# Optimization experiments

Hardware: AMD Instinct MI355X
Metric: run time of the kernel (lower is better)

## Reference

```python
import jax, jax.numpy as jnp
import numpy as np

N_CODES = 8192
EMBED_DIM = 64
N_VOXELS = 32768


def setup_inputs() -> dict:
    key = jax.random.key(0)
    k1, k2 = jax.random.split(key)
    z_feats = jax.random.normal(k1, (N_VOXELS, EMBED_DIM), dtype=jnp.float32)
    embeddings = jax.random.normal(k2, (N_CODES, EMBED_DIM), dtype=jnp.float32)
    return {"z_feats": z_feats, "embeddings": embeddings}


def reference(z_feats, embeddings):
    # Pairwise squared euclidean distances: ||z||^2 - 2 z.e + ||e||^2  [N, K]
    z_sq = jnp.sum(z_feats * z_feats, axis=1, keepdims=True)        # [N, 1]
    e_sq = jnp.sum(embeddings * embeddings, axis=1)[None, :]        # [1, K]
    d2 = z_sq - 2.0 * jnp.einsum('nd,kd->nk', z_feats, embeddings) + e_sq
    # argmin is invariant under sqrt (cdist returns sqrt, but only indices are used)
    encoding_indices = jnp.argmin(d2, axis=1)                        # [N]
    quantized_feats = embeddings[encoding_indices]                   # [N, D]
    # commitment_loss = mse(z, sg(q));  vq_loss = mse(q, sg(z)) (gradient mode)
    commitment_loss = jnp.mean((z_feats - jax.lax.stop_gradient(quantized_feats)) ** 2)
    vq_loss = jnp.mean((quantized_feats - jax.lax.stop_gradient(z_feats)) ** 2)
    # straight-through estimator
    quantized_st = z_feats + jax.lax.stop_gradient(quantized_feats - z_feats)
    indices_out = encoding_indices[:, None].astype(jnp.float32)      # [N, 1]
    return quantized_st, vq_loss, commitment_loss, indices_out
```

## Files before the change

### kernel.cpp

```cpp
#include <hip/hip_runtime.h>
#include <float.h>

#define N_VOX 32768
#define N_CODES 8192
#define DIM 64

#define Q_OFF 0
#define VQ_OFF (N_VOX * DIM)
#define CM_OFF (VQ_OFF + 1)
#define IDX_OFF (VQ_OFF + 2)

#define WS_ACC 0
#define WS_CNT 1
#define WS_ESQH 64
#define WS_IDX (WS_ESQH + N_CODES)
#define WS_EHI (WS_IDX + N_VOX)
#define WS_ELO (WS_EHI + N_CODES * DIM / 2)

typedef _Float16 half8 __attribute__((ext_vector_type(8)));
typedef float floatx4 __attribute__((ext_vector_type(4)));

__device__ inline void gld16(const void* g, void* l) {
  __builtin_amdgcn_global_load_lds(
      (const __attribute__((address_space(1))) unsigned int*)g,
      (__attribute__((address_space(3))) unsigned int*)l, 16, 0, 0);
}
__device__ inline void gld4(const void* g, void* l) {
  __builtin_amdgcn_global_load_lds(
      (const __attribute__((address_space(1))) unsigned int*)g,
      (__attribute__((address_space(3))) unsigned int*)l, 4, 0, 0);
}

__global__ __launch_bounds__(256) void k_cvt(const float* __restrict__ e,
                                             float* __restrict__ ws) {
  int gid = blockIdx.x * 256 + threadIdx.x;
  if (gid == 0) {
    ws[WS_ACC] = 0.f;
    ((int*)ws)[WS_CNT] = 0;
  }
  int row = gid >> 3, c = gid & 7;
  const float* src = e + (size_t)row * DIM + c * 8;
  float4 a = *(const float4*)src;
  float4 b = *(const float4*)(src + 4);
  float x[8] = {a.x, a.y, a.z, a.w, b.x, b.y, b.z, b.w};
  float s = 0.f;
  half8 hv, lv;
  #pragma unroll
  for (int j = 0; j < 8; ++j) {
    s += x[j] * x[j];
    _Float16 h = (_Float16)x[j];
    hv[j] = h;
    lv[j] = (_Float16)(x[j] - (float)h);
  }
  s += __shfl_xor(s, 1); s += __shfl_xor(s, 2); s += __shfl_xor(s, 4);
  if (c == 0) ws[WS_ESQH + row] = 0.5f * s;
  int p = (c + row) & 7;
  ((half8*)(ws + WS_EHI))[row * 8 + p] = hv;
  ((half8*)(ws + WS_ELO))[row * 8 + p] = lv;
}

__global__ __launch_bounds__(256, 2) void k_argmin(const float* __restrict__ z,
                                                   const float* __restrict__ e,
                                                   float* __restrict__ ws,
                                                   float* __restrict__ out) {
  __shared__ __align__(16) _Float16 sBhi[2][128 * 64];
  __shared__ __align__(16) _Float16 sBlo[2][128 * 64];
  __shared__ float sEsq[2][128];
  __shared__ float sMval[128];
  __shared__ int   sMidx[128];
  __shared__ int   sWin[64];
  __shared__ float sWsum[4];

  const int tid  = threadIdx.x;
  const int lane = tid & 63;
  const int wave = tid >> 6;
  const int n16  = lane & 15;
  const int quad = lane >> 4;
  const int vgrp = wave >> 1;
  const int chalf = wave & 1;
  const int vb = blockIdx.x * 64;

  const char* ehi_b = (const char*)(ws + WS_EHI);
  const char* elo_b = (const char*)(ws + WS_ELO);
  const char* esq_b = (const char*)(ws + WS_ESQH);

  half8 ahi[2][2], alo[2][2];
  #pragma unroll
  for (int m = 0; m < 2; ++m)
    #pragma unroll
    for (int kc = 0; kc < 2; ++kc) {
      const float* src = z + (size_t)(vb + vgrp * 32 + m * 16 + n16) * DIM
                       + kc * 32 + quad * 8;
      float4 a = *(const float4*)src;
      float4 b = *(const float4*)(src + 4);
      float x[8] = {a.x, a.y, a.z, a.w, b.x, b.y, b.z, b.w};
      #pragma unroll
      for (int j = 0; j < 8; ++j) {
        _Float16 h = (_Float16)x[j];
        ahi[m][kc][j] = h;
        alo[m][kc][j] = (_Float16)(x[j] - (float)h);
      }
    }

  float bval[2][4]; int bidx[2][4];
  #pragma unroll
  for (int m = 0; m < 2; ++m)
    #pragma unroll
    for (int r = 0; r < 4; ++r) { bval[m][r] = FLT_MAX; bidx[m][r] = 0; }

  const int s0 = ((quad + n16) & 7) * 8;
  const int s1 = ((quad + 4 + n16) & 7) * 8;

  auto stage = [&](int buf, int ct) {
    const size_t cbb = (size_t)ct * 128 * 128;
    #pragma unroll
    for (int r = 0; r < 4; ++r) {
      int off = (r * 4 + wave) * 1024;
      gld16(ehi_b + cbb + off + lane * 16, (char*)sBhi[buf] + off);
      gld16(elo_b + cbb + off + lane * 16, (char*)sBlo[buf] + off);
    }
    if (wave == 0) {
      gld4(esq_b + (size_t)ct * 512 + lane * 4, (char*)sEsq[buf]);
      gld4(esq_b + (size_t)ct * 512 + 256 + lane * 4, (char*)sEsq[buf] + 256);
    }
  };

  stage(0, 0);
  __syncthreads();

  for (int ct = 0; ct < 64; ++ct) {
    const int cur = ct & 1;
    if (ct < 63) stage(cur ^ 1, ct + 1);

    const _Float16* bhiP = sBhi[cur];
    const _Float16* bloP = sBlo[cur];
    const float*    esqP = sEsq[cur];
    const int cb = ct * 128;

    #pragma unroll
    for (int t = 0; t < 4; ++t) {
      const int row = chalf * 64 + t * 16 + n16;
      half8 bh0 = *(const half8*)&bhiP[row * 64 + s0];
      half8 bh1 = *(const half8*)&bhiP[row * 64 + s1];
      half8 bl0 = *(const half8*)&bloP[row * 64 + s0];
      half8 bl1 = *(const half8*)&bloP[row * 64 + s1];
      float eh = esqP[row];
      int code = cb + row;
      #pragma unroll
      for (int m = 0; m < 2; ++m) {
        floatx4 acc = {0.f, 0.f, 0.f, 0.f};
        acc = __builtin_amdgcn_mfma_f32_16x16x32_f16(ahi[m][0], bh0, acc, 0, 0, 0);
        acc = __builtin_amdgcn_mfma_f32_16x16x32_f16(ahi[m][1], bh1, acc, 0, 0, 0);
        acc = __builtin_amdgcn_mfma_f32_16x16x32_f16(ahi[m][0], bl0, acc, 0, 0, 0);
        acc = __builtin_amdgcn_mfma_f32_16x16x32_f16(ahi[m][1], bl1, acc, 0, 0, 0);
        acc = __builtin_amdgcn_mfma_f32_16x16x32_f16(alo[m][0], bh0, acc, 0, 0, 0);
        acc = __builtin_amdgcn_mfma_f32_16x16x32_f16(alo[m][1], bh1, acc, 0, 0, 0);
        #pragma unroll
        for (int r = 0; r < 4; ++r) {
          float tv = eh - acc[r];
          if (tv < bval[m][r]) { bval[m][r] = tv; bidx[m][r] = code; }
        }
      }
    }
    __syncthreads();
  }

  #pragma unroll
  for (int m = 0; m < 2; ++m)
    #pragma unroll
    for (int r = 0; r < 4; ++r) {
      float v = bval[m][r]; int i = bidx[m][r];
      #pragma unroll
      for (int off = 1; off < 16; off <<= 1) {
        float ov = __shfl_xor(v, off);
        int   oi = __shfl_xor(i, off);
        if (ov < v || (ov == v && oi < i)) { v = ov; i = oi; }
      }
      if (n16 == 0) {
        int vox = vgrp * 32 + m * 16 + quad * 4 + r;
        sMval[chalf * 64 + vox] = v;
        sMidx[chalf * 64 + vox] = i;
      }
    }
  __syncthreads();

  if (tid < 64) {
    float v0 = sMval[tid], v1 = sMval[64 + tid];
    int   i0 = sMidx[tid], i1 = sMidx[64 + tid];
    bool p1 = (v1 < v0) || (v1 == v0 && i1 < i0);
    int w = p1 ? i1 : i0;
    sWin[tid] = w;
    out[IDX_OFF + vb + tid] = (float)w;
  }
  __syncthreads();

  {
    const int vox = tid >> 2;
    const int dc = (tid & 3) * 16;
    const int gi = sWin[vox];
    const float* er = e + (size_t)gi * DIM + dc;
    const float* zr = z + (size_t)(vb + vox) * DIM + dc;
    float* qr = out + Q_OFF + (size_t)(vb + vox) * DIM + dc;
    float local = 0.f;
    #pragma unroll
    for (int j = 0; j < 4; ++j) {
      float4 e4 = *(const float4*)(er + j * 4);
      float4 z4 = *(const float4*)(zr + j * 4);
      *(float4*)(qr + j * 4) = e4;
      float dx = z4.x - e4.x, dy = z4.y - e4.y, dz = z4.z - e4.z, dw = z4.w - e4.w;
      local += dx * dx + dy * dy + dz * dz + dw * dw;
    }
    #pragma unroll
    for (int off = 32; off; off >>= 1) local += __shfl_xor(local, off);
    if ((tid & 63) == 0) sWsum[wave] = local;
    __syncthreads();
    if (tid == 0) {
      float bs = sWsum[0] + sWsum[1] + sWsum[2] + sWsum[3];
      atomicAdd(ws + WS_ACC, bs);
      __threadfence();
      int done = atomicAdd((int*)ws + WS_CNT, 1);
      if (done == (int)gridDim.x - 1) {
        float s = atomicAdd(ws + WS_ACC, 0.f);
        float mv = s * (1.0f / (float)(N_VOX * DIM));
        out[VQ_OFF] = mv;
        out[CM_OFF] = mv;
      }
    }
  }
}

extern "C" void kernel_launch(void* const* d_in, const int* in_sizes, int n_in,
                              void* d_out, int out_size, void* d_ws, size_t ws_size,
                              hipStream_t stream) {
  const float* z = (const float*)d_in[0];
  const float* e = (const float*)d_in[1];
  float* out = (float*)d_out;
  float* ws = (float*)d_ws;

  k_cvt<<<(N_CODES * 8) / 256, 256, 0, stream>>>(e, ws);
  k_argmin<<<N_VOX / 64, 256, 0, stream>>>(z, e, ws, out);
}
```

Before: 189.3 us.

## Split codebook across waves with direct register loads instead of LDS staging

Each wave now owns a quarter of the codebook (2048 codes) and all 64 voxels of the block. It loads split-fp16 embedding fragments straight from global memory into registers with software double-buffering, replacing the LDS staging through global_load_lds and the per-tile block barriers. The distance bias is folded into the MFMA accumulator init (-0.5||e||^2), and the selection becomes a max with a 4-way cross-wave merge at the end. This removes LDS traffic and synchronization but raises register pressure (4 voxel groups of A fragments plus two B buffers). It also leans on L2/global bandwidth, since each wave streams the codebook independently with no LDS sharing.

```diff
diff --git a/kernel.cpp b/kernel.cpp
--- a/kernel.cpp
+++ b/kernel.cpp
@@ -19,17 +19,6 @@
 
 typedef _Float16 half8 __attribute__((ext_vector_type(8)));
 typedef float floatx4 __attribute__((ext_vector_type(4)));
-
-__device__ inline void gld16(const void* g, void* l) {
-  __builtin_amdgcn_global_load_lds(
-      (const __attribute__((address_space(1))) unsigned int*)g,
-      (__attribute__((address_space(3))) unsigned int*)l, 16, 0, 0);
-}
-__device__ inline void gld4(const void* g, void* l) {
-  __builtin_amdgcn_global_load_lds(
-      (const __attribute__((address_space(1))) unsigned int*)g,
-      (__attribute__((address_space(3))) unsigned int*)l, 4, 0, 0);
-}
 
 __global__ __launch_bounds__(256) void k_cvt(const float* __restrict__ e,
                                              float* __restrict__ ws) {
@@ -54,20 +43,40 @@
   }
   s += __shfl_xor(s, 1); s += __shfl_xor(s, 2); s += __shfl_xor(s, 4);
   if (c == 0) ws[WS_ESQH + row] = 0.5f * s;
-  int p = (c + row) & 7;
-  ((half8*)(ws + WS_EHI))[row * 8 + p] = hv;
-  ((half8*)(ws + WS_ELO))[row * 8 + p] = lv;
+  ((half8*)(ws + WS_EHI))[row * 8 + c] = hv;
+  ((half8*)(ws + WS_ELO))[row * 8 + c] = lv;
+}
+
+__device__ __forceinline__ floatx4 mfma16(half8 a, half8 b, floatx4 c) {
+  return __builtin_amdgcn_mfma_f32_16x16x32_f16(a, b, c, 0, 0, 0);
+}
+
+__device__ __forceinline__ void comps(const half8 (&ahi)[4][2],
+                                      const half8 (&alo)[4][2],
+                                      half8 bh0, half8 bh1, half8 bl0, half8 bl1,
+                                      float eh, int code,
+                                      float (&bmax)[4][4], int (&bidx)[4][4]) {
+  #pragma unroll
+  for (int m = 0; m < 4; ++m) {
+    floatx4 acc = {-eh, -eh, -eh, -eh};
+    acc = mfma16(ahi[m][0], bh0, acc);
+    acc = mfma16(ahi[m][1], bh1, acc);
+    acc = mfma16(ahi[m][0], bl0, acc);
+    acc = mfma16(ahi[m][1], bl1, acc);
+    acc = mfma16(alo[m][0], bh0, acc);
+    acc = mfma16(alo[m][1], bh1, acc);
+    #pragma unroll
+    for (int r = 0; r < 4; ++r)
+      if (acc[r] > bmax[m][r]) { bmax[m][r] = acc[r]; bidx[m][r] = code; }
+  }
 }
 
 __global__ __launch_bounds__(256, 2) void k_argmin(const float* __restrict__ z,
                                                    const float* __restrict__ e,
                                                    float* __restrict__ ws,
                                                    float* __restrict__ out) {
-  __shared__ __align__(16) _Float16 sBhi[2][128 * 64];
-  __shared__ __align__(16) _Float16 sBlo[2][128 * 64];
-  __shared__ float sEsq[2][128];
-  __shared__ float sMval[128];
-  __shared__ int   sMidx[128];
+  __shared__ float sMval[4][64];
+  __shared__ int   sMidx[4][64];
   __shared__ int   sWin[64];
   __shared__ float sWsum[4];
 
@@ -76,20 +85,15 @@
   const int wave = tid >> 6;
   const int n16  = lane & 15;
   const int quad = lane >> 4;
-  const int vgrp = wave >> 1;
-  const int chalf = wave & 1;
-  const int vb = blockIdx.x * 64;
-
-  const char* ehi_b = (const char*)(ws + WS_EHI);
-  const char* elo_b = (const char*)(ws + WS_ELO);
-  const char* esq_b = (const char*)(ws + WS_ESQH);
-
-  half8 ahi[2][2], alo[2][2];
-  #pragma unroll
-  for (int m = 0; m < 2; ++m)
+  const int vb   = blockIdx.x * 64;
+  const int wcode = wave * 2048;
+
+  half8 ahi[4][2], alo[4][2];
+  #pragma unroll
+  for (int m = 0; m < 4; ++m)
     #pragma unroll
     for (int kc = 0; kc < 2; ++kc) {
-      const float* src = z + (size_t)(vb + vgrp * 32 + m * 16 + n16) * DIM
+      const float* src = z + (size_t)(vb + m * 16 + n16) * DIM
                        + kc * 32 + quad * 8;
       float4 a = *(const float4*)src;
       float4 b = *(const float4*)(src + 4);
@@ -102,95 +106,83 @@
       }
     }
 
-  float bval[2][4]; int bidx[2][4];
-  #pragma unroll
-  for (int m = 0; m < 2; ++m)
-    #pragma unroll
-    for (int r = 0; r < 4; ++r) { bval[m][r] = FLT_MAX; bidx[m][r] = 0; }
-
-  const int s0 = ((quad + n16) & 7) * 8;
-  const int s1 = ((quad + 4 + n16) & 7) * 8;
-
-  auto stage = [&](int buf, int ct) {
-    const size_t cbb = (size_t)ct * 128 * 128;
+  float bmax[4][4]; int bidx[4][4];
+  #pragma unroll
+  for (int m = 0; m < 4; ++m)
+    #pragma unroll
+    for (int r = 0; r < 4; ++r) { bmax[m][r] = -FLT_MAX; bidx[m][r] = 0; }
+
+  const char* pHi = (const char*)(ws + WS_EHI)
+                  + (size_t)(wcode + n16) * 128 + quad * 16;
+  const char* pLo = (const char*)(ws + WS_ELO)
+                  + (size_t)(wcode + n16) * 128 + quad * 16;
+  const char* pEs = (const char*)(ws + WS_ESQH) + (size_t)(wcode + n16) * 4;
+
+#define LOADT(ct, H00, H01, H10, H11, L00, L01, L10, L11, E0, E1)  \
+  {                                                                \
+    size_t o = (size_t)(ct) * 4096;                                \
+    H00 = *(const half8*)(pHi + o);                                \
+    H01 = *(const half8*)(pHi + o + 64);                           \
+    H10 = *(const half8*)(pHi + o + 2048);                         \
+    H11 = *(const half8*)(pHi + o + 2112);                         \
+    L00 = *(const half8*)(pLo + o);                                \
+    L01 = *(const half8*)(pLo + o + 64);                           \
+    L10 = *(const half8*)(pLo + o + 2048);                         \
+    L11 = *(const half8*)(pLo + o + 2112);                         \
+    E0 = *(const float*)(pEs + (size_t)(ct) * 128);                \
+    E1 = *(const float*)(pEs + (size_t)(ct) * 128 + 64);           \
+  }
+
+#define COMPT(ct, H00, H01, H10, H11, L00, L01, L10, L11, E0, E1)            \
+  {                                                                          \
+    comps(ahi, alo, H00, H01, L00, L01, E0, wcode + (ct) * 32 + n16,         \
+          bmax, bidx);                                                       \
+    comps(ahi, alo, H10, H11, L10, L11, E1, wcode + (ct) * 32 + 16 + n16,    \
+          bmax, bidx);                                                       \
+  }
+
+  half8 xh00, xh01, xh10, xh11, xl00, xl01, xl10, xl11; float xe0, xe1;
+  half8 yh00, yh01, yh10, yh11, yl00, yl01, yl10, yl11; float ye0, ye1;
+
+  LOADT(0, xh00, xh01, xh10, xh11, xl00, xl01, xl10, xl11, xe0, xe1);
+  for (int ct = 0; ct < 64; ct += 2) {
+    LOADT(ct + 1, yh00, yh01, yh10, yh11, yl00, yl01, yl10, yl11, ye0, ye1);
+    COMPT(ct, xh00, xh01, xh10, xh11, xl00, xl01, xl10, xl11, xe0, xe1);
+    if (ct + 2 < 64)
+      LOADT(ct + 2, xh00, xh01, xh10, xh11, xl00, xl01, xl10, xl11, xe0, xe1);
+    COMPT(ct + 1, yh00, yh01, yh10, yh11, yl00, yl01, yl10, yl11, ye0, ye1);
+  }
+#undef LOADT
+#undef COMPT
+
+  #pragma unroll
+  for (int m = 0; m < 4; ++m)
     #pragma unroll
     for (int r = 0; r < 4; ++r) {
-      int off = (r * 4 + wave) * 1024;
-      gld16(ehi_b + cbb + off + lane * 16, (char*)sBhi[buf] + off);
-      gld16(elo_b + cbb + off + lane * 16, (char*)sBlo[buf] + off);
-    }
-    if (wave == 0) {
-      gld4(esq_b + (size_t)ct * 512 + lane * 4, (char*)sEsq[buf]);
-      gld4(esq_b + (size_t)ct * 512 + 256 + lane * 4, (char*)sEsq[buf] + 256);
-    }
-  };
-
-  stage(0, 0);
-  __syncthreads();
-
-  for (int ct = 0; ct < 64; ++ct) {
-    const int cur = ct & 1;
-    if (ct < 63) stage(cur ^ 1, ct + 1);
-
-    const _Float16* bhiP = sBhi[cur];
-    const _Float16* bloP = sBlo[cur];
-    const float*    esqP = sEsq[cur];
-    const int cb = ct * 128;
-
-    #pragma unroll
-    for (int t = 0; t < 4; ++t) {
-      const int row = chalf * 64 + t * 16 + n16;
-      half8 bh0 = *(const half8*)&bhiP[row * 64 + s0];
-      half8 bh1 = *(const half8*)&bhiP[row * 64 + s1];
-      half8 bl0 = *(const half8*)&bloP[row * 64 + s0];
-      half8 bl1 = *(const half8*)&bloP[row * 64 + s1];
-      float eh = esqP[row];
-      int code = cb + row;
-      #pragma unroll
-      for (int m = 0; m < 2; ++m) {
-        floatx4 acc = {0.f, 0.f, 0.f, 0.f};
-        acc = __builtin_amdgcn_mfma_f32_16x16x32_f16(ahi[m][0], bh0, acc, 0, 0, 0);
-        acc = __builtin_amdgcn_mfma_f32_16x16x32_f16(ahi[m][1], bh1, acc, 0, 0, 0);
-        acc = __builtin_amdgcn_mfma_f32_16x16x32_f16(ahi[m][0], bl0, acc, 0, 0, 0);
-        acc = __builtin_amdgcn_mfma_f32_16x16x32_f16(ahi[m][1], bl1, acc, 0, 0, 0);
-        acc = __builtin_amdgcn_mfma_f32_16x16x32_f16(alo[m][0], bh0, acc, 0, 0, 0);
-        acc = __builtin_amdgcn_mfma_f32_16x16x32_f16(alo[m][1], bh1, acc, 0, 0, 0);
-        #pragma unroll
-        for (int r = 0; r < 4; ++r) {
-          float tv = eh - acc[r];
-          if (tv < bval[m][r]) { bval[m][r] = tv; bidx[m][r] = code; }
-        }
-      }
-    }
-    __syncthreads();
-  }
-
-  #pragma unroll
-  for (int m = 0; m < 2; ++m)
-    #pragma unroll
-    for (int r = 0; r < 4; ++r) {
-      float v = bval[m][r]; int i = bidx[m][r];
+      float v = bmax[m][r]; int i = bidx[m][r];
       #pragma unroll
       for (int off = 1; off < 16; off <<= 1) {
         float ov = __shfl_xor(v, off);
         int   oi = __shfl_xor(i, off);
-        if (ov < v || (ov == v && oi < i)) { v = ov; i = oi; }
+        if (ov > v || (ov == v && oi < i)) { v = ov; i = oi; }
       }
       if (n16 == 0) {
-        int vox = vgrp * 32 + m * 16 + quad * 4 + r;
-        sMval[chalf * 64 + vox] = v;
-        sMidx[chalf * 64 + vox] = i;
+        int vox = m * 16 + quad * 4 + r;
+        sMval[wave][vox] = v;
+        sMidx[wave][vox] = i;
       }
     }
   __syncthreads();
 
   if (tid < 64) {
-    float v0 = sMval[tid], v1 = sMval[64 + tid];
-    int   i0 = sMidx[tid], i1 = sMidx[64 + tid];
-    bool p1 = (v1 < v0) || (v1 == v0 && i1 < i0);
-    int w = p1 ? i1 : i0;
-    sWin[tid] = w;
-    out[IDX_OFF + vb + tid] = (float)w;
+    float v = sMval[0][tid]; int i = sMidx[0][tid];
+    #pragma unroll
+    for (int q = 1; q < 4; ++q) {
+      float ov = sMval[q][tid]; int oi = sMidx[q][tid];
+      if (ov > v || (ov == v && oi < i)) { v = ov; i = oi; }
+    }
+    sWin[tid] = i;
+    out[IDX_OFF + vb + tid] = (float)i;
   }
   __syncthreads();
 
```

After: 209.9 us. 10.9% more time.

## Split codebook across four blocks per voxel tile with atomic packed-key argmin

Applied to the files above, without the earlier changes.

Each 64-voxel tile is now handled by four blocks, each scanning a quarter of the codebook with smaller 64-code tiles and less LDS. The partial argmins are combined through a 64-bit atomicMin on a packed (value, index) key, and the last-arriving block of each group does the gather and loss. The accumulator is also initialised with -esq so the compare runs on the raw MFMA output. This targets the small grid (512 blocks) and low occupancy, at the cost of extra global atomics, a per-group arrival counter, and reloading z in all four blocks.

```diff
diff --git a/kernel.cpp b/kernel.cpp
--- a/kernel.cpp
+++ b/kernel.cpp
@@ -12,10 +12,11 @@
 
 #define WS_ACC 0
 #define WS_CNT 1
-#define WS_ESQH 64
-#define WS_IDX (WS_ESQH + N_CODES)
-#define WS_EHI (WS_IDX + N_VOX)
-#define WS_ELO (WS_EHI + N_CODES * DIM / 2)
+#define WS_GCNT 2
+#define WS_ESQH 516
+#define WS_KEY  (WS_ESQH + N_CODES)
+#define WS_EHI  (WS_KEY + 2 * N_VOX)
+#define WS_ELO  (WS_EHI + N_CODES * DIM / 2)
 
 typedef _Float16 half8 __attribute__((ext_vector_type(8)));
 typedef float floatx4 __attribute__((ext_vector_type(4)));
@@ -31,13 +32,24 @@
       (__attribute__((address_space(3))) unsigned int*)l, 4, 0, 0);
 }
 
+__device__ __forceinline__ floatx4 mfma16(half8 a, half8 b, floatx4 c) {
+  return __builtin_amdgcn_mfma_f32_16x16x32_f16(a, b, c, 0, 0, 0);
+}
+
+__device__ __forceinline__ unsigned long long packKey(float v, int code) {
+  float t = -v;
+  unsigned u = __float_as_uint(t);
+  u = (u & 0x80000000u) ? ~u : (u | 0x80000000u);
+  return ((unsigned long long)u << 32) | (unsigned)code;
+}
+
 __global__ __launch_bounds__(256) void k_cvt(const float* __restrict__ e,
                                              float* __restrict__ ws) {
   int gid = blockIdx.x * 256 + threadIdx.x;
-  if (gid == 0) {
-    ws[WS_ACC] = 0.f;
-    ((int*)ws)[WS_CNT] = 0;
-  }
+  if (gid == 0) { ws[WS_ACC] = 0.f; ((int*)ws)[WS_CNT] = 0; }
+  if (gid < 512) ((int*)ws)[WS_GCNT + gid] = 0;
+  if (gid < N_VOX) ((unsigned long long*)(ws + WS_KEY))[gid] = ~0ULL;
+
   int row = gid >> 3, c = gid & 7;
   const float* src = e + (size_t)row * DIM + c * 8;
   float4 a = *(const float4*)src;
@@ -59,17 +71,18 @@
   ((half8*)(ws + WS_ELO))[row * 8 + p] = lv;
 }
 
-__global__ __launch_bounds__(256, 2) void k_argmin(const float* __restrict__ z,
+__global__ __launch_bounds__(256, 4) void k_argmin(const float* __restrict__ z,
                                                    const float* __restrict__ e,
                                                    float* __restrict__ ws,
                                                    float* __restrict__ out) {
-  __shared__ __align__(16) _Float16 sBhi[2][128 * 64];
-  __shared__ __align__(16) _Float16 sBlo[2][128 * 64];
-  __shared__ float sEsq[2][128];
-  __shared__ float sMval[128];
-  __shared__ int   sMidx[128];
+  __shared__ __align__(16) _Float16 sBhi[2][64 * 64];
+  __shared__ __align__(16) _Float16 sBlo[2][64 * 64];
+  __shared__ float sEsq[2][64];
+  __shared__ float sMval[4][32];
+  __shared__ int   sMidx[4][32];
   __shared__ int   sWin[64];
   __shared__ float sWsum[4];
+  __shared__ int   sFin;
 
   const int tid  = threadIdx.x;
   const int lane = tid & 63;
@@ -78,11 +91,15 @@
   const int quad = lane >> 4;
   const int vgrp = wave >> 1;
   const int chalf = wave & 1;
-  const int vb = blockIdx.x * 64;
+  const int grp = blockIdx.x >> 2;
+  const int qtr = blockIdx.x & 3;
+  const int vb  = grp * 64;
+  const int cq  = qtr * 2048;
 
   const char* ehi_b = (const char*)(ws + WS_EHI);
   const char* elo_b = (const char*)(ws + WS_ELO);
   const char* esq_b = (const char*)(ws + WS_ESQH);
+  unsigned long long* keyP = (unsigned long long*)(ws + WS_KEY);
 
   half8 ahi[2][2], alo[2][2];
   #pragma unroll
@@ -102,64 +119,59 @@
       }
     }
 
-  float bval[2][4]; int bidx[2][4];
+  float bmax[2][4]; int bidx[2][4];
   #pragma unroll
   for (int m = 0; m < 2; ++m)
     #pragma unroll
-    for (int r = 0; r < 4; ++r) { bval[m][r] = FLT_MAX; bidx[m][r] = 0; }
+    for (int r = 0; r < 4; ++r) { bmax[m][r] = -FLT_MAX; bidx[m][r] = 0; }
 
   const int s0 = ((quad + n16) & 7) * 8;
   const int s1 = ((quad + 4 + n16) & 7) * 8;
 
   auto stage = [&](int buf, int ct) {
-    const size_t cbb = (size_t)ct * 128 * 128;
-    #pragma unroll
-    for (int r = 0; r < 4; ++r) {
-      int off = (r * 4 + wave) * 1024;
-      gld16(ehi_b + cbb + off + lane * 16, (char*)sBhi[buf] + off);
-      gld16(elo_b + cbb + off + lane * 16, (char*)sBlo[buf] + off);
-    }
-    if (wave == 0) {
-      gld4(esq_b + (size_t)ct * 512 + lane * 4, (char*)sEsq[buf]);
-      gld4(esq_b + (size_t)ct * 512 + 256 + lane * 4, (char*)sEsq[buf] + 256);
-    }
+    const size_t cbb = (size_t)(cq + ct * 64) * 128;
+    const int off = wave * 2048;
+    gld16(ehi_b + cbb + off + lane * 16, (char*)sBhi[buf] + off);
+    gld16(ehi_b + cbb + off + 1024 + lane * 16, (char*)sBhi[buf] + off + 1024);
+    gld16(elo_b + cbb + off + lane * 16, (char*)sBlo[buf] + off);
+    gld16(elo_b + cbb + off + 1024 + lane * 16, (char*)sBlo[buf] + off + 1024);
+    if (wave == 0)
+      gld4(esq_b + (size_t)(cq + ct * 64) * 4 + lane * 4, (char*)sEsq[buf]);
   };
 
   stage(0, 0);
   __syncthreads();
 
-  for (int ct = 0; ct < 64; ++ct) {
+  for (int ct = 0; ct < 32; ++ct) {
     const int cur = ct & 1;
-    if (ct < 63) stage(cur ^ 1, ct + 1);
+    if (ct < 31) stage(cur ^ 1, ct + 1);
 
     const _Float16* bhiP = sBhi[cur];
     const _Float16* bloP = sBlo[cur];
     const float*    esqP = sEsq[cur];
-    const int cb = ct * 128;
-
-    #pragma unroll
-    for (int t = 0; t < 4; ++t) {
-      const int row = chalf * 64 + t * 16 + n16;
+    const int cbase = cq + ct * 64;
+
+    #pragma unroll
+    for (int t = 0; t < 2; ++t) {
+      const int row = chalf * 32 + t * 16 + n16;
       half8 bh0 = *(const half8*)&bhiP[row * 64 + s0];
       half8 bh1 = *(const half8*)&bhiP[row * 64 + s1];
       half8 bl0 = *(const half8*)&bloP[row * 64 + s0];
       half8 bl1 = *(const half8*)&bloP[row * 64 + s1];
       float eh = esqP[row];
-      int code = cb + row;
+      int code = cbase + row;
       #pragma unroll
       for (int m = 0; m < 2; ++m) {
-        floatx4 acc = {0.f, 0.f, 0.f, 0.f};
-        acc = __builtin_amdgcn_mfma_f32_16x16x32_f16(ahi[m][0], bh0, acc, 0, 0, 0);
-        acc = __builtin_amdgcn_mfma_f32_16x16x32_f16(ahi[m][1], bh1, acc, 0, 0, 0);
-        acc = __builtin_amdgcn_mfma_f32_16x16x32_f16(ahi[m][0], bl0, acc, 0, 0, 0);
-        acc = __builtin_amdgcn_mfma_f32_16x16x32_f16(ahi[m][1], bl1, acc, 0, 0, 0);
-        acc = __builtin_amdgcn_mfma_f32_16x16x32_f16(alo[m][0], bh0, acc, 0, 0, 0);
-        acc = __builtin_amdgcn_mfma_f32_16x16x32_f16(alo[m][1], bh1, acc, 0, 0, 0);
+        floatx4 acc = {-eh, -eh, -eh, -eh};
+        acc = mfma16(ahi[m][0], bh0, acc);
+        acc = mfma16(ahi[m][1], bh1, acc);
+        acc = mfma16(ahi[m][0], bl0, acc);
+        acc = mfma16(ahi[m][1], bl1, acc);
+        acc = mfma16(alo[m][0], bh0, acc);
+        acc = mfma16(alo[m][1], bh1, acc);
         #pragma unroll
-        for (int r = 0; r < 4; ++r) {
-          float tv = eh - acc[r];
-          if (tv < bval[m][r]) { bval[m][r] = tv; bidx[m][r] = code; }
-        }
+        for (int r = 0; r < 4; ++r)
+          if (acc[r] > bmax[m][r]) { bmax[m][r] = acc[r]; bidx[m][r] = code; }
       }
     }
     __syncthreads();
@@ -169,31 +181,46 @@
   for (int m = 0; m < 2; ++m)
     #pragma unroll
     for (int r = 0; r < 4; ++r) {
-      float v = bval[m][r]; int i = bidx[m][r];
+      float v = bmax[m][r]; int i = bidx[m][r];
       #pragma unroll
       for (int off = 1; off < 16; off <<= 1) {
         float ov = __shfl_xor(v, off);
         int   oi = __shfl_xor(i, off);
-        if (ov < v || (ov == v && oi < i)) { v = ov; i = oi; }
+        if (ov > v || (ov == v && oi < i)) { v = ov; i = oi; }
       }
       if (n16 == 0) {
-        int vox = vgrp * 32 + m * 16 + quad * 4 + r;
-        sMval[chalf * 64 + vox] = v;
-        sMidx[chalf * 64 + vox] = i;
+        int v32 = m * 16 + quad * 4 + r;
+        sMval[wave][v32] = v;
+        sMidx[wave][v32] = i;
       }
     }
   __syncthreads();
 
   if (tid < 64) {
-    float v0 = sMval[tid], v1 = sMval[64 + tid];
-    int   i0 = sMidx[tid], i1 = sMidx[64 + tid];
-    bool p1 = (v1 < v0) || (v1 == v0 && i1 < i0);
-    int w = p1 ? i1 : i0;
-    sWin[tid] = w;
-    out[IDX_OFF + vb + tid] = (float)w;
-  }
-  __syncthreads();
-
+    int vg = tid >> 5, vi = tid & 31;
+    float v0 = sMval[vg * 2][vi],  v1 = sMval[vg * 2 + 1][vi];
+    int   i0 = sMidx[vg * 2][vi],  i1 = sMidx[vg * 2 + 1][vi];
+    bool p1 = (v1 > v0) || (v1 == v0 && i1 < i0);
+    float v = p1 ? v1 : v0;
+    int   i = p1 ? i1 : i0;
+    atomicMin(keyP + vb + tid, packKey(v, i));
+  }
+  __syncthreads();
+  if (tid == 0) {
+    __threadfence();
+    int old = atomicAdd((int*)ws + WS_GCNT + grp, 1);
+    sFin = (old == 3);
+  }
+  __syncthreads();
+  if (!sFin) return;
+
+  if (tid < 64) {
+    unsigned long long k = atomicAdd(keyP + vb + tid, 0ULL);
+    int code = (int)(unsigned)(k & 0xFFFFFFFFu);
+    sWin[tid] = code;
+    out[IDX_OFF + vb + tid] = (float)code;
+  }
+  __syncthreads();
   {
     const int vox = tid >> 2;
     const int dc = (tid & 3) * 16;
@@ -219,7 +246,7 @@
       atomicAdd(ws + WS_ACC, bs);
       __threadfence();
       int done = atomicAdd((int*)ws + WS_CNT, 1);
-      if (done == (int)gridDim.x - 1) {
+      if (done == 511) {
         float s = atomicAdd(ws + WS_ACC, 0.f);
         float mv = s * (1.0f / (float)(N_VOX * DIM));
         out[VQ_OFF] = mv;
@@ -238,5 +265,5 @@
   float* ws = (float*)d_ws;
 
   k_cvt<<<(N_CODES * 8) / 256, 256, 0, stream>>>(e, ws);
-  k_argmin<<<N_VOX / 64, 256, 0, stream>>>(z, e, ws, out);
-}
+  k_argmin<<<(N_VOX / 64) * 4, 256, 0, stream>>>(z, e, ws, out);
+}
```

New measurement: 270.9 us. +43.1%, slower.

## Halve code tile to raise occupancy, fold esq into MFMA accumulator, add setprio

Applied to the files above, without the earlier changes.

The staged codebook tile per iteration shrinks from 128 to 64 codes, halving LDS use so launch bounds can ask for 4 blocks per CU instead of 2. The loop now runs twice as many iterations. The accumulator is initialised to -esq/2, so the MFMA yields the negated score directly and the argmin becomes an argmax with no per-element subtraction. s_setprio is raised around the MFMA burst to favour math issue. The costs are twice as many barriers and stage rounds, and tighter register limits under the higher occupancy target.

```diff
diff --git a/kernel.cpp b/kernel.cpp
--- a/kernel.cpp
+++ b/kernel.cpp
@@ -29,6 +29,10 @@
   __builtin_amdgcn_global_load_lds(
       (const __attribute__((address_space(1))) unsigned int*)g,
       (__attribute__((address_space(3))) unsigned int*)l, 4, 0, 0);
+}
+
+__device__ __forceinline__ floatx4 mfma16(half8 a, half8 b, floatx4 c) {
+  return __builtin_amdgcn_mfma_f32_16x16x32_f16(a, b, c, 0, 0, 0);
 }
 
 __global__ __launch_bounds__(256) void k_cvt(const float* __restrict__ e,
@@ -59,13 +63,13 @@
   ((half8*)(ws + WS_ELO))[row * 8 + p] = lv;
 }
 
-__global__ __launch_bounds__(256, 2) void k_argmin(const float* __restrict__ z,
+__global__ __launch_bounds__(256, 4) void k_argmin(const float* __restrict__ z,
                                                    const float* __restrict__ e,
                                                    float* __restrict__ ws,
                                                    float* __restrict__ out) {
-  __shared__ __align__(16) _Float16 sBhi[2][128 * 64];
-  __shared__ __align__(16) _Float16 sBlo[2][128 * 64];
-  __shared__ float sEsq[2][128];
+  __shared__ __align__(16) _Float16 sBhi[2][64 * 64];
+  __shared__ __align__(16) _Float16 sBlo[2][64 * 64];
+  __shared__ float sEsq[2][64];
   __shared__ float sMval[128];
   __shared__ int   sMidx[128];
   __shared__ int   sWin[64];
@@ -102,65 +106,62 @@
       }
     }
 
-  float bval[2][4]; int bidx[2][4];
+  float bmax[2][4]; int bidx[2][4];
   #pragma unroll
   for (int m = 0; m < 2; ++m)
     #pragma unroll
-    for (int r = 0; r < 4; ++r) { bval[m][r] = FLT_MAX; bidx[m][r] = 0; }
+    for (int r = 0; r < 4; ++r) { bmax[m][r] = -FLT_MAX; bidx[m][r] = 0; }
 
   const int s0 = ((quad + n16) & 7) * 8;
   const int s1 = ((quad + 4 + n16) & 7) * 8;
 
   auto stage = [&](int buf, int ct) {
-    const size_t cbb = (size_t)ct * 128 * 128;
-    #pragma unroll
-    for (int r = 0; r < 4; ++r) {
-      int off = (r * 4 + wave) * 1024;
-      gld16(ehi_b + cbb + off + lane * 16, (char*)sBhi[buf] + off);
-      gld16(elo_b + cbb + off + lane * 16, (char*)sBlo[buf] + off);
-    }
-    if (wave == 0) {
-      gld4(esq_b + (size_t)ct * 512 + lane * 4, (char*)sEsq[buf]);
-      gld4(esq_b + (size_t)ct * 512 + 256 + lane * 4, (char*)sEsq[buf] + 256);
-    }
+    const size_t cbb = (size_t)ct * 64 * 128;
+    const int off = wave * 2048;
+    gld16(ehi_b + cbb + off + lane * 16, (char*)sBhi[buf] + off);
+    gld16(ehi_b + cbb + off + 1024 + lane * 16, (char*)sBhi[buf] + off + 1024);
+    gld16(elo_b + cbb + off + lane * 16, (char*)sBlo[buf] + off);
+    gld16(elo_b + cbb + off + 1024 + lane * 16, (char*)sBlo[buf] + off + 1024);
+    if (wave == 0)
+      gld4(esq_b + (size_t)ct * 256 + lane * 4, (char*)sEsq[buf]);
   };
 
   stage(0, 0);
   __syncthreads();
 
-  for (int ct = 0; ct < 64; ++ct) {
+  for (int ct = 0; ct < 128; ++ct) {
     const int cur = ct & 1;
-    if (ct < 63) stage(cur ^ 1, ct + 1);
+    if (ct < 127) stage(cur ^ 1, ct + 1);
 
     const _Float16* bhiP = sBhi[cur];
     const _Float16* bloP = sBlo[cur];
     const float*    esqP = sEsq[cur];
-    const int cb = ct * 128;
-
-    #pragma unroll
-    for (int t = 0; t < 4; ++t) {
-      const int row = chalf * 64 + t * 16 + n16;
+    const int cbase = ct * 64;
+
+    #pragma unroll
+    for (int t = 0; t < 2; ++t) {
+      const int row = chalf * 32 + t * 16 + n16;
       half8 bh0 = *(const half8*)&bhiP[row * 64 + s0];
       half8 bh1 = *(const half8*)&bhiP[row * 64 + s1];
       half8 bl0 = *(const half8*)&bloP[row * 64 + s0];
       half8 bl1 = *(const half8*)&bloP[row * 64 + s1];
       float eh = esqP[row];
-      int code = cb + row;
+      int code = cbase + row;
+      __builtin_amdgcn_s_setprio(1);
       #pragma unroll
       for (int m = 0; m < 2; ++m) {
-        floatx4 acc = {0.f, 0.f, 0.f, 0.f};
-        acc = __builtin_amdgcn_mfma_f32_16x16x32_f16(ahi[m][0], bh0, acc, 0, 0, 0);
-        acc = __builtin_amdgcn_mfma_f32_16x16x32_f16(ahi[m][1], bh1, acc, 0, 0, 0);
-        acc = __builtin_amdgcn_mfma_f32_16x16x32_f16(ahi[m][0], bl0, acc, 0, 0, 0);
-        acc = __builtin_amdgcn_mfma_f32_16x16x32_f16(ahi[m][1], bl1, acc, 0, 0, 0);
-        acc = __builtin_amdgcn_mfma_f32_16x16x32_f16(alo[m][0], bh0, acc, 0, 0, 0);
-        acc = __builtin_amdgcn_mfma_f32_16x16x32_f16(alo[m][1], bh1, acc, 0, 0, 0);
+        floatx4 acc = {-eh, -eh, -eh, -eh};
+        acc = mfma16(ahi[m][0], bh0, acc);
+        acc = mfma16(ahi[m][1], bh1, acc);
+        acc = mfma16(ahi[m][0], bl0, acc);
+        acc = mfma16(ahi[m][1], bl1, acc);
+        acc = mfma16(alo[m][0], bh0, acc);
+        acc = mfma16(alo[m][1], bh1, acc);
         #pragma unroll
-        for (int r = 0; r < 4; ++r) {
-          float tv = eh - acc[r];
-          if (tv < bval[m][r]) { bval[m][r] = tv; bidx[m][r] = code; }
-        }
-      }
+        for (int r = 0; r < 4; ++r)
+          if (acc[r] > bmax[m][r]) { bmax[m][r] = acc[r]; bidx[m][r] = code; }
+      }
+      __builtin_amdgcn_s_setprio(0);
     }
     __syncthreads();
   }
@@ -169,12 +170,12 @@
   for (int m = 0; m < 2; ++m)
     #pragma unroll
     for (int r = 0; r < 4; ++r) {
-      float v = bval[m][r]; int i = bidx[m][r];
+      float v = bmax[m][r]; int i = bidx[m][r];
       #pragma unroll
       for (int off = 1; off < 16; off <<= 1) {
         float ov = __shfl_xor(v, off);
         int   oi = __shfl_xor(i, off);
-        if (ov < v || (ov == v && oi < i)) { v = ov; i = oi; }
+        if (ov > v || (ov == v && oi < i)) { v = ov; i = oi; }
       }
       if (n16 == 0) {
         int vox = vgrp * 32 + m * 16 + quad * 4 + r;
@@ -187,7 +188,7 @@
   if (tid < 64) {
     float v0 = sMval[tid], v1 = sMval[64 + tid];
     int   i0 = sMidx[tid], i1 = sMidx[64 + tid];
-    bool p1 = (v1 < v0) || (v1 == v0 && i1 < i0);
+    bool p1 = (v1 > v0) || (v1 == v0 && i1 < i0);
     int w = p1 ? i1 : i0;
     sWin[tid] = w;
     out[IDX_OFF + vb + tid] = (float)w;
```

After: 217.0 us. 14.6% more time.
